# Kernel optimization log

Measured on AMD Instinct MI355X. Metric: run time of the kernel, lower is better.

The kernel has to match this reference:

```python
import jax, jax.numpy as jnp
import numpy as np

LN_EPS = 1e-5


def setup_inputs() -> dict:
    key = jax.random.key(0)
    ks = jax.random.split(key, 8)
    B, C, H, W = 16, 768, 64, 64
    cond_dim = 1024
    inp = {}
    inp["spatial_features"] = jax.random.normal(ks[0], (B, C, H, W), dtype=jnp.float32)
    inp["conditioning"] = jax.random.normal(ks[1], (B, cond_dim), dtype=jnp.float32)
    # conditioning_proj: Linear(cond_dim -> C)
    inp["w_cond"] = jax.random.normal(ks[2], (C, cond_dim), dtype=jnp.float32) * 0.02
    inp["b_cond"] = jnp.zeros((C,), dtype=jnp.float32)
    # MultiheadAttention packed in-projection [3C, C] and bias [3C]
    inp["in_proj_w"] = jax.random.normal(ks[3], (3 * C, C), dtype=jnp.float32) * 0.02
    inp["in_proj_b"] = jnp.zeros((3 * C,), dtype=jnp.float32)
    # MHA out_proj
    inp["attn_out_w"] = jax.random.normal(ks[4], (C, C), dtype=jnp.float32) * 0.02
    inp["attn_out_b"] = jnp.zeros((C,), dtype=jnp.float32)
    # output_proj Linear (dropout is identity at inference)
    inp["w_out"] = jax.random.normal(ks[5], (C, C), dtype=jnp.float32) * 0.02
    inp["b_out"] = jnp.zeros((C,), dtype=jnp.float32)
    # LayerNorm affine
    inp["ln_gamma"] = jnp.ones((C,), dtype=jnp.float32)
    inp["ln_beta"] = jnp.zeros((C,), dtype=jnp.float32)
    return inp


def reference(spatial_features, conditioning, w_cond, b_cond, in_proj_w, in_proj_b,
              attn_out_w, attn_out_b, w_out, b_out, ln_gamma, ln_beta):
    B, C, H, W = spatial_features.shape
    S = H * W
    # [B, C, H, W] -> [B, S, C]
    spatial_flat = spatial_features.reshape(B, C, S).transpose(0, 2, 1)
    # conditioning projection -> single KV token per batch: [B, C]
    cond = conditioning @ w_cond.T + b_cond
    # With a single key, softmax over the key axis is identically 1, so the
    # attention output is exactly the value vector broadcast over all queries;
    # Q and K projections have zero effect on output (and zero gradient).
    wv = in_proj_w[2 * C:]          # value rows of packed in-projection
    bv = in_proj_b[2 * C:]
    v = cond @ wv.T + bv            # [B, C]
    attn = v @ attn_out_w.T + attn_out_b  # MHA out_proj, [B, C]
    # output_proj (dropout = identity in eval)
    proj = attn @ w_out.T + b_out   # [B, C]
    # residual + LayerNorm over channel dim
    x = spatial_flat + proj[:, None, :]  # [B, S, C]
    mu = jnp.mean(x, axis=-1, keepdims=True)
    var = jnp.mean(jnp.square(x - mu), axis=-1, keepdims=True)
    y = (x - mu) * jax.lax.rsqrt(var + LN_EPS) * ln_gamma + ln_beta
    # [B, S, C] -> [B, C, H, W]
    return y.transpose(0, 2, 1).reshape(B, C, H, W)
```

## Files before the change

### kernel.cpp

```cpp
#include <hip/hip_runtime.h>

#define CDIM 768
#define SDIM 4096
#define SV (SDIM / 4)

typedef float nfloat4 __attribute__((ext_vector_type(4)));

__global__ __launch_bounds__(256) void small_gemm_kernel(
    const float* __restrict__ X, const float* __restrict__ W,
    const float* __restrict__ bias, float* __restrict__ out,
    int Cn, int K)
{
    int gid  = blockIdx.x * blockDim.x + threadIdx.x;
    int wid  = gid >> 6;
    int lane = threadIdx.x & 63;
    int total = 16 * Cn;
    if (wid >= total) return;
    int b = wid / Cn;
    int c = wid - b * Cn;
    const float* x = X + (size_t)b * K;
    const float* w = W + (size_t)c * K;
    float acc = 0.f;
    for (int k = lane * 4; k < K; k += 256) {
        float4 xv = *(const float4*)(x + k);
        float4 wv = *(const float4*)(w + k);
        acc += xv.x * wv.x + xv.y * wv.y + xv.z * wv.z + xv.w * wv.w;
    }
#pragma unroll
    for (int m = 32; m; m >>= 1) acc += __shfl_xor(acc, m, 64);
    if (lane == 0) out[wid] = acc + bias[c];
}

__global__ __launch_bounds__(256) void fused_add_ln_v2(
    const float* __restrict__ sp, const float* __restrict__ proj,
    const float* __restrict__ gamma, const float* __restrict__ beta,
    float* __restrict__ out)
{
    __shared__ float s_proj[CDIM], s_gamma[CDIM], s_beta[CDIM];
    __shared__ float4 red_s[4][4];
    __shared__ float4 red_q[4][4];

    const int b  = blockIdx.y;
    const int s0 = blockIdx.x * 16;
    const int t  = threadIdx.x;
    for (int i = t; i < CDIM; i += 256) {
        s_proj[i]  = proj[b * CDIM + i];
        s_gamma[i] = gamma[i];
        s_beta[i]  = beta[i];
    }
    __syncthreads();

    const int si = t & 3;
    const int cg = t >> 2;
    const int c0 = cg * (CDIM / 64);

    const float4* spv  = (const float4*)(sp  + (size_t)b * CDIM * SDIM + s0) + (size_t)c0 * SV + si;
    nfloat4*      outv = (nfloat4*)     (out + (size_t)b * CDIM * SDIM + s0) + (size_t)c0 * SV + si;

    float4 x[12];
    float4 S = make_float4(0, 0, 0, 0);
    float4 Q = make_float4(0, 0, 0, 0);
#pragma unroll
    for (int j = 0; j < 12; ++j) {
        float4 v = spv[(size_t)j * SV];
        float  p = s_proj[c0 + j];
        v.x += p; v.y += p; v.z += p; v.w += p;
        x[j] = v;
        S.x += v.x; S.y += v.y; S.z += v.z; S.w += v.w;
        Q.x += v.x * v.x; Q.y += v.y * v.y; Q.z += v.z * v.z; Q.w += v.w * v.w;
    }

#pragma unroll
    for (int m = 4; m <= 32; m <<= 1) {
        S.x += __shfl_xor(S.x, m, 64); S.y += __shfl_xor(S.y, m, 64);
        S.z += __shfl_xor(S.z, m, 64); S.w += __shfl_xor(S.w, m, 64);
        Q.x += __shfl_xor(Q.x, m, 64); Q.y += __shfl_xor(Q.y, m, 64);
        Q.z += __shfl_xor(Q.z, m, 64); Q.w += __shfl_xor(Q.w, m, 64);
    }
    const int wave = t >> 6;
    const int lane = t & 63;
    if (lane < 4) {
        red_s[wave][lane] = S;
        red_q[wave][lane] = Q;
    }
    __syncthreads();

    float4 Sa = make_float4(0, 0, 0, 0), Qa = make_float4(0, 0, 0, 0);
#pragma unroll
    for (int g = 0; g < 4; ++g) {
        float4 a = red_s[g][si], q = red_q[g][si];
        Sa.x += a.x; Sa.y += a.y; Sa.z += a.z; Sa.w += a.w;
        Qa.x += q.x; Qa.y += q.y; Qa.z += q.z; Qa.w += q.w;
    }
    const float inv = 1.f / CDIM;
    float4 mu = make_float4(Sa.x * inv, Sa.y * inv, Sa.z * inv, Sa.w * inv);
    float4 rs;
    rs.x = rsqrtf(Qa.x * inv - mu.x * mu.x + 1e-5f);
    rs.y = rsqrtf(Qa.y * inv - mu.y * mu.y + 1e-5f);
    rs.z = rsqrtf(Qa.z * inv - mu.z * mu.z + 1e-5f);
    rs.w = rsqrtf(Qa.w * inv - mu.w * mu.w + 1e-5f);

#pragma unroll
    for (int j = 0; j < 12; ++j) {
        float g  = s_gamma[c0 + j];
        float be = s_beta[c0 + j];
        nfloat4 y;
        y.x = (x[j].x - mu.x) * rs.x * g + be;
        y.y = (x[j].y - mu.y) * rs.y * g + be;
        y.z = (x[j].z - mu.z) * rs.z * g + be;
        y.w = (x[j].w - mu.w) * rs.w * g + be;
        __builtin_nontemporal_store(y, &outv[(size_t)j * SV]);
    }
}

extern "C" void kernel_launch(void* const* d_in, const int* in_sizes, int n_in,
                              void* d_out, int out_size, void* d_ws, size_t ws_size,
                              hipStream_t stream) {
    const float* sp           = (const float*)d_in[0];
    const float* conditioning = (const float*)d_in[1];
    const float* w_cond       = (const float*)d_in[2];
    const float* b_cond       = (const float*)d_in[3];
    const float* in_proj_w    = (const float*)d_in[4];
    const float* in_proj_b    = (const float*)d_in[5];
    const float* attn_out_w   = (const float*)d_in[6];
    const float* attn_out_b   = (const float*)d_in[7];
    const float* w_out        = (const float*)d_in[8];
    const float* b_out        = (const float*)d_in[9];
    const float* ln_gamma     = (const float*)d_in[10];
    const float* ln_beta      = (const float*)d_in[11];
    float* out = (float*)d_out;
    float* ws  = (float*)d_ws;

    float* cond = ws;
    float* v    = ws + 12288;
    float* attn = ws + 24576;
    float* proj = ws + 36864;

    const int gemm_blocks = (16 * CDIM) / 4;
    small_gemm_kernel<<<gemm_blocks, 256, 0, stream>>>(
        conditioning, w_cond, b_cond, cond, CDIM, 1024);
    small_gemm_kernel<<<gemm_blocks, 256, 0, stream>>>(
        cond, in_proj_w + 2 * CDIM * CDIM, in_proj_b + 2 * CDIM, v, CDIM, CDIM);
    small_gemm_kernel<<<gemm_blocks, 256, 0, stream>>>(
        v, attn_out_w, attn_out_b, attn, CDIM, CDIM);
    small_gemm_kernel<<<gemm_blocks, 256, 0, stream>>>(
        attn, w_out, b_out, proj, CDIM, CDIM);

    dim3 grid(SDIM / 16, 16);
    fused_add_ln_v2<<<grid, 256, 0, stream>>>(sp, proj, ln_gamma, ln_beta, out);
}
```

Before: 424.9 us.

## Split fused LayerNorm into stats pass and normalize pass with wider coalesced tiles

Replaces the single fused add+LayerNorm kernel with two kernels. The first computes per-position sums and sums of squares over channels into workspace, and the second re-reads the input and normalizes it, with the channel range split across a third grid dimension. The aim is long contiguous coalesced rows and low register pressure instead of narrow 16-position tiles that hold 12 float4 per thread. In exchange, the large input tensor is read twice, plus there is an extra launch and stats traffic.

```diff
diff --git a/kernel.cpp b/kernel.cpp
--- a/kernel.cpp
+++ b/kernel.cpp
@@ -2,7 +2,6 @@
 
 #define CDIM 768
 #define SDIM 4096
-#define SV (SDIM / 4)
 
 typedef float nfloat4 __attribute__((ext_vector_type(4)));
 
@@ -31,85 +30,105 @@
     if (lane == 0) out[wid] = acc + bias[c];
 }
 
-__global__ __launch_bounds__(256) void fused_add_ln_v2(
+__global__ __launch_bounds__(256) void ln_stats(
     const float* __restrict__ sp, const float* __restrict__ proj,
+    float* __restrict__ Aout, float* __restrict__ Bout)
+{
+    __shared__ float s_proj[CDIM];
+    __shared__ float2 redA[4][64];
+    __shared__ float2 redB[4][64];
+    const int b  = blockIdx.y;
+    const int s0 = blockIdx.x * 128;
+    const int t  = threadIdx.x;
+    for (int i = t; i < CDIM; i += 256) s_proj[i] = proj[b * CDIM + i];
+    __syncthreads();
+
+    const int lane = t & 63;
+    const int wave = t >> 6;
+    const float2* base = (const float2*)(sp + (size_t)b * CDIM * SDIM + s0) + lane;
+
+    float2 A = make_float2(0.f, 0.f), B = make_float2(0.f, 0.f);
+    const int cbeg = wave * (CDIM / 4);
+    for (int c = cbeg; c < cbeg + CDIM / 4; c += 8) {
+        float2 v[8];
+#pragma unroll
+        for (int k = 0; k < 8; ++k) v[k] = base[(size_t)(c + k) * (SDIM / 2)];
+#pragma unroll
+        for (int k = 0; k < 8; ++k) {
+            float p  = s_proj[c + k];
+            float ax = v[k].x + p, ay = v[k].y + p;
+            A.x += ax;      A.y += ay;
+            B.x += ax * ax; B.y += ay * ay;
+        }
+    }
+    redA[wave][lane] = A;
+    redB[wave][lane] = B;
+    __syncthreads();
+
+    if (t < 64) {
+        float2 a = redA[0][t], bb = redB[0][t];
+#pragma unroll
+        for (int w = 1; w < 4; ++w) {
+            a.x  += redA[w][t].x;  a.y  += redA[w][t].y;
+            bb.x += redB[w][t].x;  bb.y += redB[w][t].y;
+        }
+        ((float2*)(Aout + (size_t)b * SDIM + s0))[t] = a;
+        ((float2*)(Bout + (size_t)b * SDIM + s0))[t] = bb;
+    }
+}
+
+__global__ __launch_bounds__(256) void ln_norm(
+    const float* __restrict__ sp, const float* __restrict__ proj,
+    const float* __restrict__ Ain, const float* __restrict__ Bin,
     const float* __restrict__ gamma, const float* __restrict__ beta,
     float* __restrict__ out)
 {
-    __shared__ float s_proj[CDIM], s_gamma[CDIM], s_beta[CDIM];
-    __shared__ float4 red_s[4][4];
-    __shared__ float4 red_q[4][4];
-
-    const int b  = blockIdx.y;
-    const int s0 = blockIdx.x * 16;
-    const int t  = threadIdx.x;
-    for (int i = t; i < CDIM; i += 256) {
-        s_proj[i]  = proj[b * CDIM + i];
-        s_gamma[i] = gamma[i];
-        s_beta[i]  = beta[i];
+    __shared__ float s_p[CDIM / 4], s_g[CDIM / 4], s_b[CDIM / 4];
+    const int b      = blockIdx.y;
+    const int s0     = blockIdx.x * 256;
+    const int c_base = blockIdx.z * (CDIM / 4);
+    const int t      = threadIdx.x;
+    if (t < CDIM / 4) {
+        s_p[t] = proj[b * CDIM + c_base + t];
+        s_g[t] = gamma[c_base + t];
+        s_b[t] = beta[c_base + t];
     }
     __syncthreads();
 
-    const int si = t & 3;
-    const int cg = t >> 2;
-    const int c0 = cg * (CDIM / 64);
+    const int lane = t & 63;
+    const int wave = t >> 6;
 
-    const float4* spv  = (const float4*)(sp  + (size_t)b * CDIM * SDIM + s0) + (size_t)c0 * SV + si;
-    nfloat4*      outv = (nfloat4*)     (out + (size_t)b * CDIM * SDIM + s0) + (size_t)c0 * SV + si;
+    float4 A  = ((const float4*)(Ain + (size_t)b * SDIM + s0))[lane];
+    float4 Bv = ((const float4*)(Bin + (size_t)b * SDIM + s0))[lane];
+    const float inv = 1.f / CDIM;
+    float4 mu, rs;
+    mu.x = A.x * inv; mu.y = A.y * inv; mu.z = A.z * inv; mu.w = A.w * inv;
+    rs.x = rsqrtf(Bv.x * inv - mu.x * mu.x + 1e-5f);
+    rs.y = rsqrtf(Bv.y * inv - mu.y * mu.y + 1e-5f);
+    rs.z = rsqrtf(Bv.z * inv - mu.z * mu.z + 1e-5f);
+    rs.w = rsqrtf(Bv.w * inv - mu.w * mu.w + 1e-5f);
 
-    float4 x[12];
-    float4 S = make_float4(0, 0, 0, 0);
-    float4 Q = make_float4(0, 0, 0, 0);
+    const float4* spv  = (const float4*)(sp  + (size_t)b * CDIM * SDIM + s0) + lane;
+    nfloat4*      outv = (nfloat4*)     (out + (size_t)b * CDIM * SDIM + s0) + lane;
+
+    const int rbeg = wave * 48;
+    for (int r = rbeg; r < rbeg + 48; r += 4) {
+        float4 v[4];
 #pragma unroll
-    for (int j = 0; j < 12; ++j) {
-        float4 v = spv[(size_t)j * SV];
-        float  p = s_proj[c0 + j];
-        v.x += p; v.y += p; v.z += p; v.w += p;
-        x[j] = v;
-        S.x += v.x; S.y += v.y; S.z += v.z; S.w += v.w;
-        Q.x += v.x * v.x; Q.y += v.y * v.y; Q.z += v.z * v.z; Q.w += v.w * v.w;
-    }
-
+        for (int k = 0; k < 4; ++k)
+            v[k] = spv[(size_t)(c_base + r + k) * (SDIM / 4)];
 #pragma unroll
-    for (int m = 4; m <= 32; m <<= 1) {
-        S.x += __shfl_xor(S.x, m, 64); S.y += __shfl_xor(S.y, m, 64);
-        S.z += __shfl_xor(S.z, m, 64); S.w += __shfl_xor(S.w, m, 64);
-        Q.x += __shfl_xor(Q.x, m, 64); Q.y += __shfl_xor(Q.y, m, 64);
-        Q.z += __shfl_xor(Q.z, m, 64); Q.w += __shfl_xor(Q.w, m, 64);
-    }
-    const int wave = t >> 6;
-    const int lane = t & 63;
-    if (lane < 4) {
-        red_s[wave][lane] = S;
-        red_q[wave][lane] = Q;
-    }
-    __syncthreads();
-
-    float4 Sa = make_float4(0, 0, 0, 0), Qa = make_float4(0, 0, 0, 0);
-#pragma unroll
-    for (int g = 0; g < 4; ++g) {
-        float4 a = red_s[g][si], q = red_q[g][si];
-        Sa.x += a.x; Sa.y += a.y; Sa.z += a.z; Sa.w += a.w;
-        Qa.x += q.x; Qa.y += q.y; Qa.z += q.z; Qa.w += q.w;
-    }
-    const float inv = 1.f / CDIM;
-    float4 mu = make_float4(Sa.x * inv, Sa.y * inv, Sa.z * inv, Sa.w * inv);
-    float4 rs;
-    rs.x = rsqrtf(Qa.x * inv - mu.x * mu.x + 1e-5f);
-    rs.y = rsqrtf(Qa.y * inv - mu.y * mu.y + 1e-5f);
-    rs.z = rsqrtf(Qa.z * inv - mu.z * mu.z + 1e-5f);
-    rs.w = rsqrtf(Qa.w * inv - mu.w * mu.w + 1e-5f);
-
-#pragma unroll
-    for (int j = 0; j < 12; ++j) {
-        float g  = s_gamma[c0 + j];
-        float be = s_beta[c0 + j];
-        nfloat4 y;
-        y.x = (x[j].x - mu.x) * rs.x * g + be;
-        y.y = (x[j].y - mu.y) * rs.y * g + be;
-        y.z = (x[j].z - mu.z) * rs.z * g + be;
-        y.w = (x[j].w - mu.w) * rs.w * g + be;
-        __builtin_nontemporal_store(y, &outv[(size_t)j * SV]);
+        for (int k = 0; k < 4; ++k) {
+            float p  = s_p[r + k];
+            float g  = s_g[r + k];
+            float be = s_b[r + k];
+            nfloat4 y;
+            y.x = (v[k].x + p - mu.x) * rs.x * g + be;
+            y.y = (v[k].y + p - mu.y) * rs.y * g + be;
+            y.z = (v[k].z + p - mu.z) * rs.z * g + be;
+            y.w = (v[k].w + p - mu.w) * rs.w * g + be;
+            __builtin_nontemporal_store(y, &outv[(size_t)(c_base + r + k) * (SDIM / 4)]);
+        }
     }
 }
 
@@ -135,6 +154,8 @@
     float* v    = ws + 12288;
     float* attn = ws + 24576;
     float* proj = ws + 36864;
+    float* Ast  = ws + 49152;
+    float* Bst  = ws + 114688;
 
     const int gemm_blocks = (16 * CDIM) / 4;
     small_gemm_kernel<<<gemm_blocks, 256, 0, stream>>>(
@@ -146,6 +167,7 @@
     small_gemm_kernel<<<gemm_blocks, 256, 0, stream>>>(
         attn, w_out, b_out, proj, CDIM, CDIM);
 
-    dim3 grid(SDIM / 16, 16);
-    fused_add_ln_v2<<<grid, 256, 0, stream>>>(sp, proj, ln_gamma, ln_beta, out);
+    ln_stats<<<dim3(SDIM / 128, 16), 256, 0, stream>>>(sp, proj, Ast, Bst);
+    ln_norm<<<dim3(SDIM / 256, 16, 4), 256, 0, stream>>>(
+        sp, proj, Ast, Bst, ln_gamma, ln_beta, out);
 }
```

After: 411.0 us. 1.03x faster.
